# Performance work log

Hardware: AMD Instinct MI355X
Metric: run time of the kernel (lower is better)

Reference implementation:

```python
import jax, jax.numpy as jnp
import numpy as np

EPS = 1e-5

def layer_norm(x, w, b):
    mu = jnp.mean(x, axis=-1, keepdims=True)
    var = jnp.var(x, axis=-1, keepdims=True)
    return (x - mu) * jax.lax.rsqrt(var + EPS) * w + b

def setup_inputs() -> dict:
    key = jax.random.key(0)
    ks = jax.random.split(key, 9)
    B, N, d, hidden = 1, 512, 64, 128
    s = 0.02
    return {
        "z": jax.random.normal(ks[0], (B, N, N, d), dtype=jnp.float32),
        "ln_in_w": jnp.ones((d,), jnp.float32),
        "ln_in_b": jnp.zeros((d,), jnp.float32),
        "Wp": jax.random.normal(ks[1], (d, 2 * hidden), jnp.float32) * s,
        "Wg": jax.random.normal(ks[2], (d, 2 * hidden), jnp.float32) * s,
        "ln_out_w": jnp.ones((hidden,), jnp.float32),
        "ln_out_b": jnp.zeros((hidden,), jnp.float32),
        "Wout": jax.random.normal(ks[3], (hidden, d), jnp.float32) * s,
        "Wgate": jax.random.normal(ks[4], (d, d), jnp.float32) * s,
    }

def reference(z, ln_in_w, ln_in_b, Wp, Wg, ln_out_w, ln_out_b, Wout, Wgate):
    # z: [B, N, N, d]
    h = layer_norm(z, ln_in_w, ln_in_b)
    p = h @ Wp                               # [B,N,N,2*hidden]
    g_in = jax.nn.sigmoid(h @ Wg)            # [B,N,N,2*hidden]
    pg = p * g_in
    a, b = jnp.split(pg, 2, axis=-1)         # each [B,N,N,hidden]
    # direction == 'outgoing'
    out = jnp.einsum('bikd,bjkd->bijd', a, b)  # [B,N,N,hidden]
    out = layer_norm(out, ln_out_w, ln_out_b)
    g_out = jax.nn.sigmoid(h @ Wgate)        # [B,N,N,d]
    return (out @ Wout) * g_out              # [B,N,N,d]
```

## Files before the change

kernel.cpp:

```cpp
#include <hip/hip_runtime.h>
#include <hip/hip_fp16.h>


typedef _Float16 half_t;
typedef _Float16 f16x4 __attribute__((ext_vector_type(4)));
typedef _Float16 f16x8 __attribute__((ext_vector_type(8)));
typedef float f32x4 __attribute__((ext_vector_type(4)));

#define NSEQ 512
#define HID 128
#define ROWS (NSEQ * NSEQ)

#define GLOAD16(src, dst)                                                        \
    __builtin_amdgcn_global_load_lds(                                            \
        (const __attribute__((address_space(1))) void*)(src),                    \
        (__attribute__((address_space(3))) void*)(dst), 16, 0, 0)

__device__ __forceinline__ float fast_sigmoid(float x) {
    float e = __builtin_amdgcn_exp2f(-1.44269504088896f * x);
    return __builtin_amdgcn_rcpf(1.f + e);
}

__global__ void k_prep_w(const float* __restrict__ Wp, const float* __restrict__ Wg,
                         const float* __restrict__ Wgate,
                         const float* __restrict__ ln_out_w, const float* __restrict__ ln_out_b,
                         const float* __restrict__ Wout,
                         half_t* __restrict__ Wimg, half_t* __restrict__ W1t,
                         float* __restrict__ s1, float* __restrict__ s2) {
    int bid = blockIdx.x, t = threadIdx.x;
    if (bid < 18) {
        int chunk = bid * 256 + t;
        int ch = chunk >= 2304;
        int q = chunk - ch * 2304;
        int lr = q >> 3, slot = q & 7;
        int co = slot ^ (lr & 7);
        int grow;
        if (lr < 128)      grow = ch * 128 + lr;
        else if (lr < 256) grow = 256 + ch * 128 + (lr - 128);
        else               grow = 512 + ch * 32 + (lr - 256);
        f16x8 vals;
        #pragma unroll
        for (int j = 0; j < 8; ++j) {
            int l = co * 8 + j;
            float v;
            if (grow < 256)      v = Wp[l * 256 + grow];
            else if (grow < 512) v = Wg[l * 256 + (grow - 256)];
            else                 v = Wgate[l * 64 + (grow - 512)];
            vals[j] = (half_t)v;
        }
        *(f16x8*)(Wimg + (size_t)chunk * 8) = vals;
    } else {
        #pragma unroll
        for (int i = 0; i < 32; ++i) {
            int idx = t * 32 + i;
            int o = idx >> 7, c = idx & 127;
            W1t[idx] = (half_t)(ln_out_w[c] * Wout[c * 64 + o]);
        }
        if (t < 64) {
            float a1 = 0.f, a2 = 0.f;
            for (int c = 0; c < 128; ++c) {
                float wo = Wout[c * 64 + t];
                a1 += ln_out_w[c] * wo;
                a2 += ln_out_b[c] * wo;
            }
            s1[t] = a1; s2[t] = a2;
        }
    }
}

__global__ __launch_bounds__(256) void k_ln_in(const float* __restrict__ z,
                                               const float* __restrict__ w,
                                               const float* __restrict__ b,
                                               half_t* __restrict__ h) {
    int t = threadIdx.x;
    int row = blockIdx.x * 16 + (t >> 4);
    int c4 = t & 15;
    f32x4 x = *(const f32x4*)(z + (size_t)row * 64 + c4 * 4);
    float s = x[0] + x[1] + x[2] + x[3];
    float s2 = x[0]*x[0] + x[1]*x[1] + x[2]*x[2] + x[3]*x[3];
    #pragma unroll
    for (int off = 1; off < 16; off <<= 1) {
        s  += __shfl_xor(s,  off, 64);
        s2 += __shfl_xor(s2, off, 64);
    }
    float mu = s * (1.f / 64.f);
    float var = s2 * (1.f / 64.f) - mu * mu;
    float rs = rsqrtf(var + 1e-5f);
    f32x4 wv = *(const f32x4*)(w + c4 * 4);
    f32x4 bv = *(const f32x4*)(b + c4 * 4);
    f16x4 o;
    #pragma unroll
    for (int j = 0; j < 4; ++j)
        o[j] = (half_t)((x[j] - mu) * rs * wv[j] + bv[j]);
    *(f16x4*)(h + (size_t)row * 64 + c4 * 4) = o;
}

__global__ __launch_bounds__(256) void k_proj(const half_t* __restrict__ h,
                                              const half_t* __restrict__ Wimg,
                                              half_t* __restrict__ a_t,
                                              half_t* __restrict__ b_t,
                                              half_t* __restrict__ g_out) {
    __shared__ half_t Wl[288 * 64];
    __shared__ half_t pgl[64 * 66];

    int t = threadIdx.x;
    int ch = blockIdx.y;
    int bx = blockIdx.x;
    int r0 = bx * 64;
    int wid = t >> 6, lane = t & 63;
    int m = lane & 15, g = lane >> 4;

    const half_t* wsrc = Wimg + (size_t)ch * 2304 * 8;
    #pragma unroll
    for (int it = 0; it < 9; ++it) {
        int cb = it * 256 + wid * 64;
        GLOAD16(wsrc + (size_t)(cb + lane) * 8, Wl + (size_t)cb * 8);
    }

    int growbase = r0 + wid * 16;
    f16x8 af[2];
    #pragma unroll
    for (int ks = 0; ks < 2; ++ks)
        af[ks] = *(const f16x8*)(h + (size_t)(growbase + m) * 64 + ks * 32 + g * 8);

    __syncthreads();

    half_t* dst = (ch == 0) ? a_t : b_t;
    int swz = (bx >> 4) & 3;

    for (int grp = 0; grp < 2; ++grp) {
        #pragma unroll
        for (int pt4 = 0; pt4 < 4; ++pt4) {
            int pt = grp * 4 + pt4;
            f32x4 accp = {0.f, 0.f, 0.f, 0.f}, accg = {0.f, 0.f, 0.f, 0.f};
            #pragma unroll
            for (int ks = 0; ks < 2; ++ks) {
                int kb = (ks * 32 + g * 8) * 2;
                int lrp = pt * 16 + m;
                f16x8 bp = *(const f16x8*)((char*)Wl + lrp * 128 + (kb ^ ((lrp & 7) << 4)));
                int lrg = 128 + pt * 16 + m;
                f16x8 bg = *(const f16x8*)((char*)Wl + lrg * 128 + (kb ^ ((lrg & 7) << 4)));
                accp = __builtin_amdgcn_mfma_f32_16x16x32_f16(af[ks], bp, accp, 0, 0, 0);
                accg = __builtin_amdgcn_mfma_f32_16x16x32_f16(af[ks], bg, accg, 0, 0, 0);
            }
            f16x4 pk;
            #pragma unroll
            for (int r = 0; r < 4; ++r)
                pk[r] = (half_t)(accp[r] * fast_sigmoid(accg[r]));
            *(f16x4*)&pgl[(pt4 * 16 + m) * 66 + wid * 16 + g * 4] = pk;
        }
        __syncthreads();
        #pragma unroll
        for (int it = 0; it < 2; ++it) {
            int chunk = it * 256 + t;
            int cl = chunk >> 3, r8 = chunk & 7;
            f16x8 v = *(const f16x8*)&pgl[cl * 66 + r8 * 8];
            int dk = (r8 & 4) | ((r8 & 3) ^ swz);
            *(f16x8*)(dst + (size_t)(grp * 64 + cl) * ROWS + r0 + dk * 8) = v;
        }
        __syncthreads();
    }

    for (int gt = 0; gt < 2; ++gt) {
        f32x4 acc = {0.f, 0.f, 0.f, 0.f};
        #pragma unroll
        for (int ks = 0; ks < 2; ++ks) {
            int kb = (ks * 32 + g * 8) * 2;
            int lr = 256 + gt * 16 + m;
            f16x8 bb = *(const f16x8*)((char*)Wl + lr * 128 + (kb ^ ((lr & 7) << 4)));
            acc = __builtin_amdgcn_mfma_f32_16x16x32_f16(af[ks], bb, acc, 0, 0, 0);
        }
        int och = ch * 32 + gt * 16 + m;
        #pragma unroll
        for (int r = 0; r < 4; ++r) {
            float og = fast_sigmoid(acc[r]);
            int grow = growbase + g * 4 + r;
            g_out[(size_t)grow * 64 + och] = (half_t)og;
        }
    }
}

__global__ __launch_bounds__(256) void k_einsum(const half_t* __restrict__ a_t,
                                                const half_t* __restrict__ b_t,
                                                half_t* __restrict__ out_mid) {
    __shared__ half_t lds[4][3][6144];

    int t = threadIdx.x;
    int wid = t >> 6, lane = t & 63;
    int m = lane & 15, g = lane >> 4;

    int bid = blockIdx.x;
    int xcd = bid & 7;
    int r = bid >> 3;
    int tt = r & 7, u = r >> 3;
    int c = xcd + 8 * u;
    int id = tt * 4 + wid;
    int i0 = (id >> 3) * 128, j0 = (id & 7) * 64;

    const half_t* A = a_t + (size_t)c * ROWS;
    const half_t* B = b_t + (size_t)c * ROWS;

    f32x4 acc[8][4] = {};

#define STAGE(ktt, bi)                                                            \
    {                                                                             \
        half_t* dA = &lds[wid][bi][0];                                            \
        half_t* dB = &lds[wid][bi][4096];                                         \
        _Pragma("unroll")                                                         \
        for (int inst = 0; inst < 8; ++inst) {                                    \
            int q = inst * 64 + lane;                                             \
            GLOAD16(A + (size_t)(i0 + (q >> 2)) * 512 + (ktt) * 32 + (q & 3) * 8, \
                    dA + (size_t)inst * 512);                                     \
        }                                                                         \
        _Pragma("unroll")                                                         \
        for (int inst = 0; inst < 4; ++inst) {                                    \
            int q = inst * 64 + lane;                                             \
            GLOAD16(B + (size_t)(j0 + (q >> 2)) * 512 + (ktt) * 32 + (q & 3) * 8, \
                    dB + (size_t)inst * 512);                                     \
        }                                                                         \
    }

    STAGE(0, 0);
    STAGE(1, 1);

    #pragma unroll
    for (int kt = 0; kt < 16; ++kt) {
        const int cur = kt % 3;
        if (kt < 14) {
            STAGE(kt + 2, (kt + 2) % 3);
            asm volatile("s_waitcnt vmcnt(24)" ::: "memory");
        } else if (kt == 14) {
            asm volatile("s_waitcnt vmcnt(12)" ::: "memory");
        } else {
            asm volatile("s_waitcnt vmcnt(0)" ::: "memory");
        }
        __builtin_amdgcn_sched_barrier(0);

        const half_t* Ac = &lds[wid][cur][0];
        const half_t* Bc = &lds[wid][cur][4096];
        f16x8 bf[4];
        #pragma unroll
        for (int ni = 0; ni < 4; ++ni) {
            int lrow = ni * 16 + m;
            bf[ni] = *(const f16x8*)((const char*)Bc + lrow * 64 +
                                     ((g ^ ((lrow >> 1) & 3)) << 4));
        }
        #pragma unroll
        for (int mi = 0; mi < 8; ++mi) {
            int lrow = mi * 16 + m;
            f16x8 afr = *(const f16x8*)((const char*)Ac + lrow * 64 +
                                        ((g ^ ((lrow >> 1) & 3)) << 4));
            #pragma unroll
            for (int ni = 0; ni < 4; ++ni)
                acc[mi][ni] = __builtin_amdgcn_mfma_f32_16x16x32_f16(afr, bf[ni], acc[mi][ni], 0, 0, 0);
        }
    }
#undef STAGE

    half_t* O = out_mid + (size_t)c * ROWS;
    #pragma unroll
    for (int mi = 0; mi < 8; ++mi) {
        #pragma unroll
        for (int ni = 0; ni < 4; ++ni) {
            int row = i0 + mi * 16 + g * 4;
            int col = j0 + ni * 16 + m;
            #pragma unroll
            for (int r2 = 0; r2 < 4; ++r2)
                O[(size_t)(row + r2) * 512 + col] = (half_t)acc[mi][ni][r2];
        }
    }
}

__global__ __launch_bounds__(256) void k_final(const half_t* __restrict__ out_mid,
                                               const half_t* __restrict__ W1t,
                                               const float* __restrict__ s1g,
                                               const float* __restrict__ s2g,
                                               const half_t* __restrict__ g_out,
                                               float* __restrict__ out) {
    __shared__ half_t midl[128 * 64];
    __shared__ half_t midt[64 * 128];
    __shared__ half_t w1l[64 * 128];
    __shared__ half_t gl[64 * 72];
    __shared__ float smu[64], srs[64], s1l[64], s2l[64];

    int t = threadIdx.x;
    int pos0 = blockIdx.x * 64;

    #pragma unroll
    for (int it = 0; it < 4; ++it) {
        int chunk = it * 256 + t;
        int cc = chunk >> 3, co = chunk & 7;
        *(uint4*)((char*)midl + cc * 128 + co * 16) =
            *(const uint4*)(out_mid + (size_t)cc * ROWS + pos0 + co * 8);
    }
    #pragma unroll
    for (int it = 0; it < 4; ++it) {
        int chunk = it * 256 + t;
        int row = chunk >> 4, slot = chunk & 15;
        *(uint4*)((char*)w1l + row * 256 + ((slot * 16) ^ ((row & 7) << 4))) =
            *(const uint4*)(W1t + row * 128 + slot * 8);
    }
    #pragma unroll
    for (int it = 0; it < 2; ++it) {
        int chunk = it * 256 + t;
        int row = chunk >> 3, co = chunk & 7;
        *(uint4*)((char*)gl + row * 144 + co * 16) =
            *(const uint4*)(g_out + (size_t)(pos0 + row) * 64 + co * 8);
    }
    if (t < 64) { s1l[t] = s1g[t]; s2l[t] = s2g[t]; }
    __syncthreads();

    {
        int p = t >> 2, q = t & 3;
        float s = 0.f, s2 = 0.f;
        #pragma unroll
        for (int cc4 = 0; cc4 < 4; ++cc4) {
            f16x8 pack;
            #pragma unroll
            for (int j = 0; j < 8; ++j) {
                half_t hv = midl[(q * 32 + cc4 * 8 + j) * 64 + p];
                float v = (float)hv;
                s += v; s2 += v * v;
                pack[j] = hv;
            }
            int slot = q * 4 + cc4;
            *(f16x8*)((char*)midt + p * 256 + ((slot * 16) ^ ((p & 7) << 4))) = pack;
        }
        s  += __shfl_xor(s, 1, 64);  s  += __shfl_xor(s, 2, 64);
        s2 += __shfl_xor(s2, 1, 64); s2 += __shfl_xor(s2, 2, 64);
        if (q == 0) {
            float mu = s * (1.f / 128.f);
            float var = s2 * (1.f / 128.f) - mu * mu;
            smu[p] = mu;
            srs[p] = rsqrtf(var + 1e-5f);
        }
    }
    __syncthreads();

    int wid = t >> 6, lane = t & 63;
    int m = lane & 15, g = lane >> 4;

    f32x4 acc[4] = {};
    #pragma unroll
    for (int ks = 0; ks < 4; ++ks) {
        int arow = wid * 16 + m;
        f16x8 af = *(const f16x8*)((char*)midt + arow * 256 +
                                   (((4 * ks + g) * 16) ^ ((arow & 7) << 4)));
        #pragma unroll
        for (int ni = 0; ni < 4; ++ni) {
            int brow = ni * 16 + m;
            f16x8 bf = *(const f16x8*)((char*)w1l + brow * 256 +
                                       (((4 * ks + g) * 16) ^ ((brow & 7) << 4)));
            acc[ni] = __builtin_amdgcn_mfma_f32_16x16x32_f16(af, bf, acc[ni], 0, 0, 0);
        }
    }

    #pragma unroll
    for (int ni = 0; ni < 4; ++ni) {
        int o = ni * 16 + m;
        float v1 = s1l[o], v2 = s2l[o];
        #pragma unroll
        for (int r = 0; r < 4; ++r) {
            int lrow = wid * 16 + g * 4 + r;
            float mu = smu[lrow], rs = srs[lrow];
            float val = acc[ni][r] * rs - mu * rs * v1 + v2;
            float gate = (float)gl[lrow * 72 + o];
            out[(size_t)(pos0 + lrow) * 64 + o] = val * gate;
        }
    }
}

extern "C" void kernel_launch(void* const* d_in, const int* in_sizes, int n_in,
                              void* d_out, int out_size, void* d_ws, size_t ws_size,
                              hipStream_t stream) {
    const float* z        = (const float*)d_in[0];
    const float* ln_in_w  = (const float*)d_in[1];
    const float* ln_in_b  = (const float*)d_in[2];
    const float* Wp       = (const float*)d_in[3];
    const float* Wg       = (const float*)d_in[4];
    const float* ln_out_w = (const float*)d_in[5];
    const float* ln_out_b = (const float*)d_in[6];
    const float* Wout     = (const float*)d_in[7];
    const float* Wgate    = (const float*)d_in[8];
    float* out = (float*)d_out;

    char* wsb = (char*)d_ws;
    half_t* Wimg = (half_t*)wsb;
    half_t* W1t  = (half_t*)(wsb + 81920);
    float*  s1   = (float*)(wsb + 98304);
    float*  s2   = (float*)(wsb + 98560);
    half_t* a_t  = (half_t*)(wsb + 131072);
    half_t* b_t  = a_t + (size_t)HID * ROWS;
    half_t* gout = b_t + (size_t)HID * ROWS;
    half_t* omid = gout + (size_t)ROWS * 64;
    half_t* h    = omid;

    k_prep_w<<<dim3(19), dim3(256), 0, stream>>>(Wp, Wg, Wgate, ln_out_w, ln_out_b, Wout,
                                                 Wimg, W1t, s1, s2);
    k_ln_in<<<dim3(ROWS / 16), dim3(256), 0, stream>>>(z, ln_in_w, ln_in_b, h);
    k_proj<<<dim3(ROWS / 64, 2), dim3(256), 0, stream>>>(h, Wimg, a_t, b_t, gout);
    k_einsum<<<dim3(1024), dim3(256), 0, stream>>>(a_t, b_t, omid);
    k_final<<<dim3(ROWS / 64), dim3(256), 0, stream>>>(omid, W1t, s1, s2, gout, out);
}
```

Before: 167.1 us.

## Share LDS tiles across waves in einsum with block-level 256x128 tiling

The einsum kernel is restructured so all four waves of a block cooperatively load one shared 256x128 output tile into LDS, instead of each wave staging its own private 128x64 tile. This cuts redundant global loads and raises data reuse per block. Prefetch loads for stage k+2 are interleaved with the MFMA loop, and s_setprio is raised around the MFMAs. The cost is a block-wide barrier every k-step, and launch bounds now request two blocks per CU.

```diff
diff --git a/kernel.cpp b/kernel.cpp
--- a/kernel.cpp
+++ b/kernel.cpp
@@ -180,10 +180,11 @@
     }
 }
 
-__global__ __launch_bounds__(256) void k_einsum(const half_t* __restrict__ a_t,
-                                                const half_t* __restrict__ b_t,
-                                                half_t* __restrict__ out_mid) {
-    __shared__ half_t lds[4][3][6144];
+#define BUFH 12288
+__global__ __launch_bounds__(256, 2) void k_einsum(const half_t* __restrict__ a_t,
+                                                   const half_t* __restrict__ b_t,
+                                                   half_t* __restrict__ out_mid) {
+    __shared__ half_t lds[3 * BUFH];
 
     int t = threadIdx.x;
     int wid = t >> 6, lane = t & 63;
@@ -191,79 +192,92 @@
 
     int bid = blockIdx.x;
     int xcd = bid & 7;
-    int r = bid >> 3;
-    int tt = r & 7, u = r >> 3;
-    int c = xcd + 8 * u;
-    int id = tt * 4 + wid;
-    int i0 = (id >> 3) * 128, j0 = (id & 7) * 64;
+    int idx = bid >> 3;
+    int c = xcd + 8 * (idx >> 3);
+    int tt = idx & 7;
+    int i0 = (tt & 1) * 256, j0 = (tt >> 1) * 128;
 
     const half_t* A = a_t + (size_t)c * ROWS;
     const half_t* B = b_t + (size_t)c * ROWS;
 
+    int wr = wid >> 1, wc = wid & 1;
+
     f32x4 acc[8][4] = {};
 
-#define STAGE(ktt, bi)                                                            \
+#define STAGE_A(ktt, base, it)                                                    \
     {                                                                             \
-        half_t* dA = &lds[wid][bi][0];                                            \
-        half_t* dB = &lds[wid][bi][4096];                                         \
-        _Pragma("unroll")                                                         \
-        for (int inst = 0; inst < 8; ++inst) {                                    \
-            int q = inst * 64 + lane;                                             \
-            GLOAD16(A + (size_t)(i0 + (q >> 2)) * 512 + (ktt) * 32 + (q & 3) * 8, \
-                    dA + (size_t)inst * 512);                                     \
-        }                                                                         \
-        _Pragma("unroll")                                                         \
-        for (int inst = 0; inst < 4; ++inst) {                                    \
-            int q = inst * 64 + lane;                                             \
-            GLOAD16(B + (size_t)(j0 + (q >> 2)) * 512 + (ktt) * 32 + (q & 3) * 8, \
-                    dB + (size_t)inst * 512);                                     \
-        }                                                                         \
-    }
-
-    STAGE(0, 0);
-    STAGE(1, 1);
+        int cb = (it) * 256 + wid * 64;              \
+        int chunk = cb + lane;                                                    \
+        GLOAD16(A + (size_t)(i0 + (chunk >> 2)) * 512 + (ktt) * 32 + (chunk & 3) * 8, \
+                (base) + (size_t)cb * 8);                                         \
+    }
+#define STAGE_B(ktt, base, it)                                                    \
+    {                                                                             \
+        int cb = (it) * 256 + wid * 64;                                           \
+        int chunk = cb + lane;                                                    \
+        GLOAD16(B + (size_t)(j0 + (chunk >> 2)) * 512 + (ktt) * 32 + (chunk & 3) * 8, \
+                (base) + 8192 + (size_t)cb * 8);                                  \
+    }
+#define STAGE_ALL(ktt, base)                                                      \
+    STAGE_A(ktt, base, 0) STAGE_A(ktt, base, 1) STAGE_A(ktt, base, 2)             \
+    STAGE_A(ktt, base, 3) STAGE_B(ktt, base, 0) STAGE_B(ktt, base, 1)
+
+    STAGE_ALL(0, lds)
+    STAGE_ALL(1, lds + BUFH)
 
     #pragma unroll
     for (int kt = 0; kt < 16; ++kt) {
-        const int cur = kt % 3;
-        if (kt < 14) {
-            STAGE(kt + 2, (kt + 2) % 3);
-            asm volatile("s_waitcnt vmcnt(24)" ::: "memory");
-        } else if (kt == 14) {
-            asm volatile("s_waitcnt vmcnt(12)" ::: "memory");
-        } else {
-            asm volatile("s_waitcnt vmcnt(0)" ::: "memory");
-        }
+        const half_t* Ac = lds + (kt % 3) * BUFH;
+        const half_t* Bc = Ac + 8192;
+        half_t* nxt = lds + ((kt + 2) % 3) * BUFH;
+
+        if (kt <= 14) asm volatile("s_waitcnt vmcnt(6)" ::: "memory");
+        else          asm volatile("s_waitcnt vmcnt(0)" ::: "memory");
+        __builtin_amdgcn_s_barrier();
         __builtin_amdgcn_sched_barrier(0);
 
-        const half_t* Ac = &lds[wid][cur][0];
-        const half_t* Bc = &lds[wid][cur][4096];
         f16x8 bf[4];
         #pragma unroll
         for (int ni = 0; ni < 4; ++ni) {
-            int lrow = ni * 16 + m;
+            int lrow = wc * 64 + ni * 16 + m;
             bf[ni] = *(const f16x8*)((const char*)Bc + lrow * 64 +
                                      ((g ^ ((lrow >> 1) & 3)) << 4));
         }
-        #pragma unroll
-        for (int mi = 0; mi < 8; ++mi) {
-            int lrow = mi * 16 + m;
-            f16x8 afr = *(const f16x8*)((const char*)Ac + lrow * 64 +
-                                        ((g ^ ((lrow >> 1) & 3)) << 4));
+
+        #pragma unroll
+        for (int q = 0; q < 4; ++q) {
+            int lr0 = wr * 128 + (q * 2) * 16 + m;
+            int lr1 = lr0 + 16;
+            f16x8 af0 = *(const f16x8*)((const char*)Ac + lr0 * 64 +
+                                        ((g ^ ((lr0 >> 1) & 3)) << 4));
+            f16x8 af1 = *(const f16x8*)((const char*)Ac + lr1 * 64 +
+                                        ((g ^ ((lr1 >> 1) & 3)) << 4));
+            if (kt < 14) {
+                if (q == 0)      { STAGE_A(kt + 2, nxt, 0) STAGE_A(kt + 2, nxt, 1) }
+                else if (q == 1) { STAGE_A(kt + 2, nxt, 2) STAGE_A(kt + 2, nxt, 3) }
+                else if (q == 2) { STAGE_B(kt + 2, nxt, 0) }
+                else             { STAGE_B(kt + 2, nxt, 1) }
+            }
+            __builtin_amdgcn_s_setprio(1);
             #pragma unroll
-            for (int ni = 0; ni < 4; ++ni)
-                acc[mi][ni] = __builtin_amdgcn_mfma_f32_16x16x32_f16(afr, bf[ni], acc[mi][ni], 0, 0, 0);
-        }
-    }
-#undef STAGE
+            for (int ni = 0; ni < 4; ++ni) {
+                acc[q * 2][ni]     = __builtin_amdgcn_mfma_f32_16x16x32_f16(af0, bf[ni], acc[q * 2][ni], 0, 0, 0);
+                acc[q * 2 + 1][ni] = __builtin_amdgcn_mfma_f32_16x16x32_f16(af1, bf[ni], acc[q * 2 + 1][ni], 0, 0, 0);
+            }
+            __builtin_amdgcn_s_setprio(0);
+        }
+    }
+#undef STAGE_ALL
+#undef STAGE_B
+#undef STAGE_A
 
     half_t* O = out_mid + (size_t)c * ROWS;
     #pragma unroll
     for (int mi = 0; mi < 8; ++mi) {
         #pragma unroll
         for (int ni = 0; ni < 4; ++ni) {
-            int row = i0 + mi * 16 + g * 4;
-            int col = j0 + ni * 16 + m;
+            int row = i0 + wr * 128 + mi * 16 + g * 4;
+            int col = j0 + wc * 64 + ni * 16 + m;
             #pragma unroll
             for (int r2 = 0; r2 < 4; ++r2)
                 O[(size_t)(row + r2) * 512 + col] = (half_t)acc[mi][ni][r2];
```

Measured after the change: 157.1 us. 1.06x faster.
